# Kernel tuning notes

Hardware: AMD Instinct MI355X
Metric: run time of the kernel (lower is better)

## Reference

```python
import jax, jax.numpy as jnp
import numpy as np

MAX_DUR = 4      # durations sampled in [0, 4], so padded output len = Tmax * MAX_DUR
PAD_VALUE = 0.0  # LengthRegulator pad_value


def setup_inputs() -> dict:
    key = jax.random.key(0)
    k1, k2 = jax.random.split(key)
    B, T, D = 16, 1024, 384
    xs = jax.random.normal(k1, (B, T, D), dtype=jnp.float32)
    ds = jax.random.randint(k2, (B, T), 0, MAX_DUR + 1, dtype=jnp.int32)
    return {"xs": xs, "ds": ds}


def reference(xs, ds):
    """Duration-based repeat-interleave + pad (FastSpeech length regulator).

    Equivalent math to: [repeat_interleave(x, d, dim=0) for x, d in zip(xs, ds)]
    followed by pad_list(..., pad_value), except the padded length is the static
    capacity T*MAX_DUR instead of the data-dependent batch max (extra columns
    are pure pad_value). For output frame t of sample b, the source token is
    the i with cumsum(ds)[b, i-1] <= t < cumsum(ds)[b, i].
    """
    B, T, D = xs.shape
    out_len = T * MAX_DUR  # static output capacity

    cs = jnp.cumsum(ds, axis=1)                      # (B, T) cumulative durations
    t = jnp.arange(out_len, dtype=cs.dtype)          # (out_len,)
    # source index per output frame: count of cumsums <= t
    idx = jax.vmap(lambda c: jnp.searchsorted(c, t, side="right"))(cs)  # (B, out_len)
    valid = t[None, :] < cs[:, -1:]                  # (B, out_len) within total length
    idx = jnp.minimum(idx, T - 1)

    gathered = jnp.take_along_axis(xs, idx[:, :, None], axis=1)  # (B, out_len, D)
    return jnp.where(valid[:, :, None], gathered, jnp.asarray(PAD_VALUE, xs.dtype))
```

## Files before the change

### kernel.cpp

```cpp
#include <hip/hip_runtime.h>
#include <hip/hip_bf16.h>

#define B_SZ 16
#define T_SZ 1024
#define D_SZ 384
#define MAX_DUR 4
#define OUT_LEN (T_SZ * MAX_DUR)

__global__ __launch_bounds__(256) void cumsum_kernel(const int* __restrict__ ds,
                                                     int* __restrict__ cs) {
    __shared__ int sums[256];
    const int b   = blockIdx.x;
    const int tid = threadIdx.x;

    int4 v = ((const int4*)(ds + b * T_SZ))[tid];
    const int s0 = v.x;
    const int s1 = s0 + v.y;
    const int s2 = s1 + v.z;
    const int s3 = s2 + v.w;

    sums[tid] = s3;
    __syncthreads();

    int val = s3;
    for (int off = 1; off < 256; off <<= 1) {
        int other = (tid >= off) ? sums[tid - off] : 0;
        __syncthreads();
        val += other;
        sums[tid] = val;
        __syncthreads();
    }

    const int excl = val - s3;
    int4 o;
    o.x = excl + s0;
    o.y = excl + s1;
    o.z = excl + s2;
    o.w = excl + s3;
    ((int4*)(cs + b * T_SZ))[tid] = o;
}

__global__ __launch_bounds__(384) void regulate_kernel(const float* __restrict__ xs,
                                                       const int* __restrict__ cs,
                                                       float* __restrict__ out) {
    __shared__ int sidx[4];
    const int tid = threadIdx.x;
    const int lf  = tid / 96;
    const int col = tid - lf * 96;

    const long long fbase = (long long)blockIdx.x * 4;
    const int b = (int)(fbase >> 12);

    if (col == 0) {
        const int t = (int)(fbase & (OUT_LEN - 1)) + lf;
        const int* c = cs + b * T_SZ;
        const int total = c[T_SZ - 1];
        int idx;
        if (t >= total) {
            idx = -1;
        } else {
            int lo = 0, hi = T_SZ;
            while (lo < hi) {
                const int mid = (lo + hi) >> 1;
                if (c[mid] <= t) lo = mid + 1; else hi = mid;
            }
            idx = lo;
        }
        sidx[lf] = idx;
    }
    __syncthreads();

    const int idx = sidx[lf];
    float4 v = make_float4(0.0f, 0.0f, 0.0f, 0.0f);
    if (idx >= 0) {
        v = ((const float4*)(xs + ((long long)b * T_SZ + idx) * D_SZ))[col];
    }
    const long long f = fbase + lf;
    ((float4*)(out + f * D_SZ))[col] = v;
}

extern "C" void kernel_launch(void* const* d_in, const int* in_sizes, int n_in,
                              void* d_out, int out_size, void* d_ws, size_t ws_size,
                              hipStream_t stream) {
    const float* xs = (const float*)d_in[0];
    const int*   ds = (const int*)d_in[1];
    float*       out = (float*)d_out;
    int*         cs  = (int*)d_ws;

    cumsum_kernel<<<B_SZ, 256, 0, stream>>>(ds, cs);

    const int frames = B_SZ * OUT_LEN;
    regulate_kernel<<<frames / 4, 384, 0, stream>>>(xs, cs, out);
}
```

Baseline: 144.6 us.

## Precompute per-frame source indices by scatter instead of per-frame binary search

The prep kernel now keeps the cumulative sums in shared memory and scatters each token index into a per-frame index array, filling frames past the total length with -1. The regulate kernel then reads one index per frame rather than running a serial binary search and a block barrier. This removes about ten dependent global loads per frame and the __syncthreads from the bandwidth-bound copy kernel. In exchange the prep kernel writes a 256KB index array from only 16 blocks with uneven per-thread loops, and the workspace must hold B*OUT_LEN ints.

Result: faster. 132.5 us (-8.4%).

```diff
diff --git a/kernel.cpp b/kernel.cpp
--- a/kernel.cpp
+++ b/kernel.cpp
@@ -7,9 +7,10 @@
 #define MAX_DUR 4
 #define OUT_LEN (T_SZ * MAX_DUR)
 
-__global__ __launch_bounds__(256) void cumsum_kernel(const int* __restrict__ ds,
-                                                     int* __restrict__ cs) {
+__global__ __launch_bounds__(256) void prep_kernel(const int* __restrict__ ds,
+                                                   int* __restrict__ idxArr) {
     __shared__ int sums[256];
+    __shared__ int cs[T_SZ + 1];
     const int b   = blockIdx.x;
     const int tid = threadIdx.x;
 
@@ -32,63 +33,54 @@
     }
 
     const int excl = val - s3;
-    int4 o;
-    o.x = excl + s0;
-    o.y = excl + s1;
-    o.z = excl + s2;
-    o.w = excl + s3;
-    ((int4*)(cs + b * T_SZ))[tid] = o;
+    if (tid == 0) cs[0] = 0;
+    cs[4 * tid + 1] = excl + s0;
+    cs[4 * tid + 2] = excl + s1;
+    cs[4 * tid + 3] = excl + s2;
+    cs[4 * tid + 4] = excl + s3;
+    __syncthreads();
+
+    const int total = cs[T_SZ];
+    int* row = idxArr + b * OUT_LEN;
+
+    #pragma unroll
+    for (int j = 0; j < 4; ++j) {
+        const int i  = 4 * tid + j;
+        const int st = cs[i];
+        const int en = cs[i + 1];
+        for (int t = st; t < en; ++t) row[t] = i;
+    }
+    for (int t = total + tid; t < OUT_LEN; t += 256) row[t] = -1;
 }
 
 __global__ __launch_bounds__(384) void regulate_kernel(const float* __restrict__ xs,
-                                                       const int* __restrict__ cs,
+                                                       const int* __restrict__ idxArr,
                                                        float* __restrict__ out) {
-    __shared__ int sidx[4];
     const int tid = threadIdx.x;
     const int lf  = tid / 96;
     const int col = tid - lf * 96;
 
-    const long long fbase = (long long)blockIdx.x * 4;
-    const int b = (int)(fbase >> 12);
+    const long long f = (long long)blockIdx.x * 4 + lf;
+    const int b = (int)(f >> 12);
 
-    if (col == 0) {
-        const int t = (int)(fbase & (OUT_LEN - 1)) + lf;
-        const int* c = cs + b * T_SZ;
-        const int total = c[T_SZ - 1];
-        int idx;
-        if (t >= total) {
-            idx = -1;
-        } else {
-            int lo = 0, hi = T_SZ;
-            while (lo < hi) {
-                const int mid = (lo + hi) >> 1;
-                if (c[mid] <= t) lo = mid + 1; else hi = mid;
-            }
-            idx = lo;
-        }
-        sidx[lf] = idx;
-    }
-    __syncthreads();
-
-    const int idx = sidx[lf];
+    const int idx = idxArr[f];
     float4 v = make_float4(0.0f, 0.0f, 0.0f, 0.0f);
     if (idx >= 0) {
         v = ((const float4*)(xs + ((long long)b * T_SZ + idx) * D_SZ))[col];
     }
-    const long long f = fbase + lf;
     ((float4*)(out + f * D_SZ))[col] = v;
 }
 
 extern "C" void kernel_launch(void* const* d_in, const int* in_sizes, int n_in,
                               void* d_out, int out_size, void* d_ws, size_t ws_size,
                               hipStream_t stream) {
-    const float* xs = (const float*)d_in[0];
-    const int*   ds = (const int*)d_in[1];
+    const float* xs  = (const float*)d_in[0];
+    const int*   ds  = (const int*)d_in[1];
     float*       out = (float*)d_out;
-    int*         cs  = (int*)d_ws;
+    int*         idxArr = (int*)d_ws;
 
-    cumsum_kernel<<<B_SZ, 256, 0, stream>>>(ds, cs);
+    prep_kernel<<<B_SZ, 256, 0, stream>>>(ds, idxArr);
 
     const int frames = B_SZ * OUT_LEN;
-    regulate_kernel<<<frames / 4, 384, 0, stream>>>(xs, cs, out);
+    regulate_kernel<<<frames / 4, 384, 0, stream>>>(xs, idxArr, out);
 }
```
